# Kernel tuning notes

Hardware: AMD Instinct MI355X
Metric: run time of the kernel (lower is better)

## Reference

```python
import jax, jax.numpy as jnp
import numpy as np

B, C, H, W = 256, 256, 16, 16   # batch, backbone channels, spatial (H*W = 256 = loop count)
E, NCLS = 128, 200              # opt.embed_size, opt.class_num

def _conv(x, w, stride, pad):
    # NCHW / OIHW conv, explicit torch-style symmetric padding
    return jax.lax.conv_general_dilated(x, w, (stride, stride), [(pad, pad), (pad, pad)],
                                        dimension_numbers=('NCHW', 'OIHW', 'NCHW'))

def _bn(x, s, b):
    # eval-mode BatchNorm folded to per-channel scale + shift
    return x * s[None, :, None, None] + b[None, :, None, None]

def setup_inputs() -> dict:
    key = jax.random.key(0)
    ks = jax.random.split(key, 12)
    f = lambda k, shape, scale: jax.random.normal(k, shape, jnp.float32) * scale
    bn_s = lambda k, n: 1.0 + 0.05 * jax.random.normal(k, (n,), jnp.float32)
    bn_b = lambda k, n: 0.05 * jax.random.normal(k, (n,), jnp.float32)
    return {
        'x': f(ks[0], (B, C, H, W), 1.0),
        'embed_w': f(ks[1], (E, C), 0.05),
        'embed_b': f(ks[2], (E,), 0.05),
        'b1_conv1': f(ks[3], (512, 256, 3, 3), 0.03),
        'b1_bn1_s': bn_s(jax.random.fold_in(key, 101), 512),
        'b1_bn1_b': bn_b(jax.random.fold_in(key, 102), 512),
        'b1_conv2': f(ks[4], (512, 512, 3, 3), 0.02),
        'b1_bn2_s': bn_s(jax.random.fold_in(key, 103), 512),
        'b1_bn2_b': bn_b(jax.random.fold_in(key, 104), 512),
        'b1_down_w': f(ks[5], (512, 256, 1, 1), 0.05),
        'b1_down_s': bn_s(jax.random.fold_in(key, 105), 512),
        'b1_down_b': bn_b(jax.random.fold_in(key, 106), 512),
        'b2_conv1': f(ks[6], (512, 512, 3, 3), 0.02),
        'b2_bn1_s': bn_s(jax.random.fold_in(key, 107), 512),
        'b2_bn1_b': bn_b(jax.random.fold_in(key, 108), 512),
        'b2_conv2': f(ks[7], (512, 512, 3, 3), 0.02),
        'b2_bn2_s': bn_s(jax.random.fold_in(key, 109), 512),
        'b2_bn2_b': bn_b(jax.random.fold_in(key, 110), 512),
        'head_w': f(ks[8], (NCLS, 512), 0.05),
    }

def reference(x, embed_w, embed_b,
              b1_conv1, b1_bn1_s, b1_bn1_b, b1_conv2, b1_bn2_s, b1_bn2_b,
              b1_down_w, b1_down_s, b1_down_b,
              b2_conv1, b2_bn1_s, b2_bn1_b, b2_conv2, b2_bn2_s, b2_bn2_b,
              head_w):
    # --- resblock = resnet layer4 (two BasicBlocks, 256->512, stride 2) ---
    y = jax.nn.relu(_bn(_conv(x, b1_conv1, 2, 1), b1_bn1_s, b1_bn1_b))
    y = _bn(_conv(y, b1_conv2, 1, 1), b1_bn2_s, b1_bn2_b)
    sc = _bn(_conv(x, b1_down_w, 2, 0), b1_down_s, b1_down_b)
    y = jax.nn.relu(y + sc)                              # [B,512,8,8]
    z = jax.nn.relu(_bn(_conv(y, b2_conv1, 1, 1), b2_bn1_s, b2_bn1_b))
    z = _bn(_conv(z, b2_conv2, 1, 1), b2_bn2_s, b2_bn2_b)
    z = jax.nn.relu(z + y)
    # --- class prediction: global avg pool + bias-free linear ---
    feat = jnp.mean(z, axis=(2, 3))                      # [B,512]
    prediction = feat @ head_w.T                         # [B,NCLS]
    # --- consistency: 1x1-conv embedding, then pairwise Gram + sigmoid ---
    emb = jnp.einsum('bchw,ec->behw', x, embed_w) + embed_b[None, :, None, None]
    emb = emb.reshape(B, E, H * W)                       # [B,E,256]
    inv_sqrt_e = jnp.float32(1.0 / np.sqrt(E))
    # vol[b,q,i] = sum_c emb[b,c,i]*emb[b,c,q] / sqrt(E)  (matches the 256-iter loop)
    vol = jax.nn.sigmoid(jnp.einsum('bei,beq->bqi', emb, emb) * inv_sqrt_e)
    return (prediction, vol)
```

## Files before the change

kernel.cpp:

```cpp
#include <hip/hip_runtime.h>


using short8 = __attribute__((ext_vector_type(8))) short;
using f32x4  = __attribute__((ext_vector_type(4))) float;
typedef unsigned short u16;
typedef unsigned int   u32;

#define MFMA(a,b,c) __builtin_amdgcn_mfma_f32_16x16x32_bf16((a),(b),(c),0,0,0)

__device__ __forceinline__ u16 f2b(float f){
    u32 u = __builtin_bit_cast(u32, f);
    u += 0x7FFFu + ((u >> 16) & 1u);
    return (u16)(u >> 16);
}
__device__ __forceinline__ float b2f(u16 h){
    u32 u = ((u32)h) << 16;
    return __builtin_bit_cast(float, u);
}
__device__ __forceinline__ u32 pack2(float a, float b){
    return (u32)f2b(a) | ((u32)f2b(b) << 16);
}
__device__ __forceinline__ float sigmoidf_(float v){
    return 1.0f / (1.0f + __expf(-v));
}

__global__ __launch_bounds__(256)
void prep_kernel(const float* __restrict__ w1, const float* __restrict__ s1,
                 const float* __restrict__ w2, const float* __restrict__ s2,
                 const float* __restrict__ w3, const float* __restrict__ s3,
                 const float* __restrict__ w4, const float* __restrict__ s4,
                 const float* __restrict__ wd, const float* __restrict__ sd,
                 const float* __restrict__ ew,
                 u16* __restrict__ wp1, u16* __restrict__ wp2,
                 u16* __restrict__ wp3, u16* __restrict__ wp4,
                 u16* __restrict__ wpd, u16* __restrict__ wpe)
{
    const int N2 = 9*16*512*40, N1 = 9*8*512*40, ND = 8*512*40, NE = 8*128*40;
    int t = blockIdx.x * 256 + threadIdx.x;
    if (t < N2) {
        int j = t % 40; int r = t / 40; int co = r & 511; int q = r >> 9;
        int cc = q & 15; int dydx = q >> 4;
        float v = (j < 32) ? w2[(co*512 + cc*32 + j)*9 + dydx] * s2[co] : 0.f;
        wp2[t] = f2b(v); return;
    }
    t -= N2;
    if (t < N2) {
        int j = t % 40; int r = t / 40; int co = r & 511; int q = r >> 9;
        int cc = q & 15; int dydx = q >> 4;
        float v = (j < 32) ? w3[(co*512 + cc*32 + j)*9 + dydx] * s3[co] : 0.f;
        wp3[t] = f2b(v); return;
    }
    t -= N2;
    if (t < N2) {
        int j = t % 40; int r = t / 40; int co = r & 511; int q = r >> 9;
        int cc = q & 15; int dydx = q >> 4;
        float v = (j < 32) ? w4[(co*512 + cc*32 + j)*9 + dydx] * s4[co] : 0.f;
        wp4[t] = f2b(v); return;
    }
    t -= N2;
    if (t < N1) {
        int j = t % 40; int r = t / 40; int co = r & 511; int q = r >> 9;
        int cc = q & 7; int dydx = q >> 3;
        float v = (j < 32) ? w1[(co*256 + cc*32 + j)*9 + dydx] * s1[co] : 0.f;
        wp1[t] = f2b(v); return;
    }
    t -= N1;
    if (t < ND) {
        int j = t % 40; int r = t / 40; int co = r & 511; int cc = r >> 9;
        float v = (j < 32) ? wd[co*256 + cc*32 + j] * sd[co] : 0.f;
        wpd[t] = f2b(v); return;
    }
    t -= ND;
    if (t < NE) {
        int j = t % 40; int r = t / 40; int e = r & 127; int cc = r >> 7;
        float v = (j < 32) ? ew[e*256 + cc*32 + j] : 0.f;
        wpe[t] = f2b(v);
    }
}

__global__ __launch_bounds__(512, 2)
void conv1_kernel(const float* __restrict__ x, const u16* __restrict__ wp,
                  const float* __restrict__ bnb, u16* __restrict__ out)
{
    const int cot = blockIdx.x;
    const int b0  = blockIdx.y * 2;
    const int tid = threadIdx.x;
    const int wid = tid >> 6, lane = tid & 63;
    const int ln = lane & 15, kg = lane >> 4;
    const int wco = wid >> 1;
    const int bb  = wid & 1;

    __shared__ u16 actb[2][2*289*40];

    {
        short8 zz = {0,0,0,0,0,0,0,0};
        short8* ab = (short8*)&actb[0][0];
        for (int j = tid; j < 2*2*289*40/8; j += 512) ab[j] = zz;
    }
    __syncthreads();

    auto stage_act = [&](int cc, int p){
        #pragma unroll
        for (int it = 0; it < 16; ++it){
            int f = it*512 + tid;
            int bb2 = f >> 12; int rem = f & 4095;
            int cip = rem >> 8; int px = rem & 255;
            const float* src = &x[(((size_t)(b0+bb2)*256 + cc*32 + 2*cip)*256) + px];
            float v0 = src[0], v1 = src[256];
            int r = ((px >> 4) + 1)*17 + (px & 15) + 1;
            *(u32*)&actb[p][(bb2*289 + r)*40 + 2*cip] = pack2(v0, v1);
        }
    };

    stage_act(0, 0);
    __syncthreads();

    f32x4 zero4 = {0.f,0.f,0.f,0.f};
    f32x4 acc[4][4];
    #pragma unroll
    for (int mf = 0; mf < 4; ++mf)
        #pragma unroll
        for (int nf = 0; nf < 4; ++nf) acc[mf][nf] = zero4;

    int bbase[4];
    #pragma unroll
    for (int nf = 0; nf < 4; ++nf){
        int px = nf*16 + ln;
        bbase[nf] = (bb*289 + 34*(px>>3) + 2*(px&7))*40 + kg*8;
    }

    for (int cc = 0; cc < 8; ++cc){
        if (cc < 7) stage_act(cc+1, (cc+1) & 1);
        const u16* abp = actb[cc & 1];
        #pragma unroll
        for (int d = 0; d < 9; ++d){
            const u16* wdp = wp + ((size_t)(d*8 + cc)*512 + cot*256)*40;
            int dy = d/3, dx = d - dy*3;
            int shift = (dy*17 + dx)*40;
            short8 A[4];
            #pragma unroll
            for (int mf = 0; mf < 4; ++mf)
                A[mf] = *(const short8*)&wdp[(wco*64 + mf*16 + ln)*40 + kg*8];
            #pragma unroll
            for (int nf = 0; nf < 4; ++nf){
                short8 B = *(const short8*)&abp[bbase[nf] + shift];
                #pragma unroll
                for (int mf = 0; mf < 4; ++mf)
                    acc[mf][nf] = MFMA(A[mf], B, acc[mf][nf]);
            }
        }
        __syncthreads();
    }

    #pragma unroll
    for (int mf = 0; mf < 4; ++mf){
        int co0 = cot*256 + wco*64 + mf*16 + kg*4;
        float4 bv = *(const float4*)&bnb[co0];
        #pragma unroll
        for (int nf = 0; nf < 4; ++nf){
            int px = nf*16 + ln;
            size_t o = (((size_t)(b0+bb)*64) + px)*512 + co0;
            f32x4 a = acc[mf][nf];
            ushort4 st;
            st.x = f2b(fmaxf(a[0] + bv.x, 0.f));
            st.y = f2b(fmaxf(a[1] + bv.y, 0.f));
            st.z = f2b(fmaxf(a[2] + bv.z, 0.f));
            st.w = f2b(fmaxf(a[3] + bv.w, 0.f));
            *(ushort4*)&out[o] = st;
        }
    }
}

template<int DOWN, int RES>
__global__ __launch_bounds__(128, 3)
void conv_s1_kernel(const u16* __restrict__ in, const u16* __restrict__ wp,
                    const float* __restrict__ bnb,
                    const float* __restrict__ x, const u16* __restrict__ wpd,
                    const float* __restrict__ dbb,
                    const u16* __restrict__ res, u16* __restrict__ out)
{
    const int b   = blockIdx.x;
    const int cot = blockIdx.y;
    const int tid = threadIdx.x;
    const int wid = tid >> 6;
    const int lane = tid & 63;
    const int ln = lane & 15, kg = lane >> 4;

    __shared__ u16 actb[2][100*40];

    {
        short8 zz = {0,0,0,0,0,0,0,0};
        short8* ab = (short8*)&actb[0][0];
        for (int j = tid; j < 2*100*40/8; j += 128) ab[j] = zz;
    }
    __syncthreads();

    const int j0 = tid, j1 = 128 + tid;
    const int px0 = j0 >> 2, cg0 = j0 & 3;
    const int px1 = j1 >> 2, cg1 = j1 & 3;
    const int ld0 = (((px0>>3)+1)*10 + (px0&7) + 1)*40 + cg0*8;
    const int ld1 = (((px1>>3)+1)*10 + (px1&7) + 1)*40 + cg1*8;

    short8 sreg0, sreg1;
    auto stage_load = [&](int cc){
        sreg0 = *(const short8*)&in[(((size_t)b*64 + px0)*512) + cc*32 + cg0*8];
        sreg1 = *(const short8*)&in[(((size_t)b*64 + px1)*512) + cc*32 + cg1*8];
    };
    auto stage_store = [&](int p){
        *(short8*)&actb[p][ld0] = sreg0;
        *(short8*)&actb[p][ld1] = sreg1;
    };

    stage_load(0); stage_store(0);
    __syncthreads();

    f32x4 zero4 = {0.f,0.f,0.f,0.f};
    f32x4 acc[4][4];
    #pragma unroll
    for (int mf = 0; mf < 4; ++mf)
        #pragma unroll
        for (int nf = 0; nf < 4; ++nf) acc[mf][nf] = zero4;

    int bro[4];
    #pragma unroll
    for (int nf = 0; nf < 4; ++nf){
        int px = nf*16 + ln;
        bro[nf] = ((px>>3)*10 + (px&7))*40 + kg*8;
    }
    const int aoff = ln*40 + kg*8;
    const int abase = (cot*128 + wid*64)*40;

    for (int cc = 0; cc < 16; ++cc){
        if (cc < 15) stage_load(cc+1);
        const u16* abp = actb[cc & 1];
        #pragma unroll
        for (int dy = 0; dy < 3; ++dy){
            short8 A[3][4];
            #pragma unroll
            for (int dx = 0; dx < 3; ++dx){
                const u16* wdp = wp + (size_t)((dy*3+dx)*16 + cc)*512*40 + abase;
                #pragma unroll
                for (int mf = 0; mf < 4; ++mf)
                    A[dx][mf] = *(const short8*)&wdp[mf*640 + aoff];
            }
            #pragma unroll
            for (int dx = 0; dx < 3; ++dx){
                int shift = (dy*10 + dx)*40;
                #pragma unroll
                for (int nf = 0; nf < 4; ++nf){
                    short8 B = *(const short8*)&abp[bro[nf] + shift];
                    #pragma unroll
                    for (int mf = 0; mf < 4; ++mf)
                        acc[mf][nf] = MFMA(A[dx][mf], B, acc[mf][nf]);
                }
            }
        }
        if (cc < 15){
            stage_store((cc+1) & 1);
            __syncthreads();
        }
    }

    if (DOWN){
        for (int dc = 0; dc < 8; ++dc){
            __syncthreads();
            #pragma unroll
            for (int it = 0; it < 8; ++it){
                int f = it*128 + tid;
                int cip = f >> 6, px2 = f & 63;
                int ipx = (px2>>3)*32 + (px2&7)*2;
                const float* src = &x[(((size_t)b*256 + dc*32 + 2*cip)*256) + ipx];
                *(u32*)&actb[0][px2*40 + cip*2] = pack2(src[0], src[256]);
            }
            __syncthreads();
            const u16* wdp = wpd + (size_t)(dc*512)*40 + abase;
            short8 A[4];
            #pragma unroll
            for (int mf = 0; mf < 4; ++mf)
                A[mf] = *(const short8*)&wdp[mf*640 + aoff];
            #pragma unroll
            for (int nf = 0; nf < 4; ++nf){
                int rd = nf*16 + ln;
                short8 B = *(const short8*)&actb[0][rd*40 + kg*8];
                #pragma unroll
                for (int mf = 0; mf < 4; ++mf)
                    acc[mf][nf] = MFMA(A[mf], B, acc[mf][nf]);
            }
        }
    }

    #pragma unroll
    for (int mf = 0; mf < 4; ++mf){
        int co0 = cot*128 + wid*64 + mf*16 + kg*4;
        float4 bv = *(const float4*)&bnb[co0];
        if (DOWN){
            float4 dv = *(const float4*)&dbb[co0];
            bv.x += dv.x; bv.y += dv.y; bv.z += dv.z; bv.w += dv.w;
        }
        #pragma unroll
        for (int nf = 0; nf < 4; ++nf){
            int px = nf*16 + ln;
            size_t o = (((size_t)b*64) + px)*512 + co0;
            f32x4 a = acc[mf][nf];
            float v0 = a[0] + bv.x, v1 = a[1] + bv.y;
            float v2 = a[2] + bv.z, v3 = a[3] + bv.w;
            if (RES){
                ushort4 rv = *(const ushort4*)&res[o];
                v0 += b2f(rv.x); v1 += b2f(rv.y); v2 += b2f(rv.z); v3 += b2f(rv.w);
            }
            ushort4 st;
            st.x = f2b(fmaxf(v0, 0.f)); st.y = f2b(fmaxf(v1, 0.f));
            st.z = f2b(fmaxf(v2, 0.f)); st.w = f2b(fmaxf(v3, 0.f));
            *(ushort4*)&out[o] = st;
        }
    }
}

__global__ __launch_bounds__(256)
void head_kernel(const u16* __restrict__ z, const float* __restrict__ hw,
                 float* __restrict__ pred)
{
    const int b = blockIdx.x, tid = threadIdx.x;
    __shared__ float feat[512];
    float s0 = 0.f, s1 = 0.f;
    for (int px = 0; px < 64; ++px){
        u32 u = *(const u32*)&z[(((size_t)b*64 + px)*512) + 2*tid];
        s0 += b2f((u16)(u & 0xFFFF));
        s1 += b2f((u16)(u >> 16));
    }
    feat[2*tid]   = s0 * (1.f/64.f);
    feat[2*tid+1] = s1 * (1.f/64.f);
    __syncthreads();
    if (tid < 200){
        float acc = 0.f;
        const float4* hp = (const float4*)&hw[(size_t)tid*512];
        #pragma unroll 8
        for (int i = 0; i < 128; ++i){
            float4 h = hp[i];
            float4 f = *(const float4*)&feat[i*4];
            acc += h.x*f.x + h.y*f.y + h.z*f.z + h.w*f.w;
        }
        pred[b*200 + tid] = acc;
    }
}

__global__ __launch_bounds__(512, 2)
void gram_kernel(const float* __restrict__ x, const u16* __restrict__ wpe,
                 const float* __restrict__ eb, float* __restrict__ vol)
{
    const int b = blockIdx.x, tid = threadIdx.x;
    const int wid = tid >> 6, lane = tid & 63;
    const int ln = lane & 15, kg = lane >> 4;

    __shared__ u16 embl[256*136];
    __shared__ u16 xbl[256*40];
    __shared__ u16 ewl[128*40];

    f32x4 zero4 = {0.f,0.f,0.f,0.f};
    f32x4 ae[8][2];
    #pragma unroll
    for (int mf = 0; mf < 8; ++mf){ ae[mf][0] = zero4; ae[mf][1] = zero4; }

    for (int cc = 0; cc < 8; ++cc){
        __syncthreads();
        #pragma unroll
        for (int it = 0; it < 8; ++it){
            int f = it*512 + tid;
            int cip = f >> 8, px = f & 255;
            const float* src = &x[(((size_t)b*256 + cc*32 + 2*cip)*256) + px];
            *(u32*)&xbl[px*40 + 2*cip] = pack2(src[0], src[256]);
        }
        for (int j = tid; j < 640; j += 512)
            *(short8*)&ewl[j*8] = *(const short8*)&wpe[(cc*128)*40 + j*8];
        __syncthreads();
        short8 A[8];
        #pragma unroll
        for (int mf = 0; mf < 8; ++mf)
            A[mf] = *(const short8*)&ewl[(mf*16 + ln)*40 + kg*8];
        #pragma unroll
        for (int nf = 0; nf < 2; ++nf){
            short8 B = *(const short8*)&xbl[(wid*32 + nf*16 + ln)*40 + kg*8];
            #pragma unroll
            for (int mf = 0; mf < 8; ++mf)
                ae[mf][nf] = MFMA(A[mf], B, ae[mf][nf]);
        }
    }
    #pragma unroll
    for (int mf = 0; mf < 8; ++mf){
        int e0 = mf*16 + kg*4;
        float4 bv = *(const float4*)&eb[e0];
        #pragma unroll
        for (int nf = 0; nf < 2; ++nf){
            int px = wid*32 + nf*16 + ln;
            f32x4 a = ae[mf][nf];
            ushort4 st;
            st.x = f2b(a[0] + bv.x); st.y = f2b(a[1] + bv.y);
            st.z = f2b(a[2] + bv.z); st.w = f2b(a[3] + bv.w);
            *(ushort4*)&embl[px*136 + e0] = st;
        }
    }
    __syncthreads();

    const int wq = wid >> 2, wi = wid & 3;
    f32x4 g[8][4];
    #pragma unroll
    for (int mf = 0; mf < 8; ++mf)
        #pragma unroll
        for (int nf = 0; nf < 4; ++nf) g[mf][nf] = zero4;

    #pragma unroll
    for (int ks = 0; ks < 4; ++ks){
        short8 A[8];
        #pragma unroll
        for (int mf = 0; mf < 8; ++mf)
            A[mf] = *(const short8*)&embl[(wq*128 + mf*16 + ln)*136 + ks*32 + kg*8];
        #pragma unroll
        for (int nf = 0; nf < 4; ++nf){
            short8 B = *(const short8*)&embl[(wi*64 + nf*16 + ln)*136 + ks*32 + kg*8];
            #pragma unroll
            for (int mf = 0; mf < 8; ++mf)
                g[mf][nf] = MFMA(A[mf], B, g[mf][nf]);
        }
    }
    const float sc = 0.08838834764831845f;
    #pragma unroll
    for (int mf = 0; mf < 8; ++mf){
        #pragma unroll
        for (int nf = 0; nf < 4; ++nf){
            int i = wi*64 + nf*16 + ln;
            #pragma unroll
            for (int r = 0; r < 4; ++r){
                int q = wq*128 + mf*16 + kg*4 + r;
                vol[(((size_t)b*256 + q)*256) + i] = sigmoidf_(g[mf][nf][r] * sc);
            }
        }
    }
}

extern "C" void kernel_launch(void* const* d_in, const int* in_sizes, int n_in,
                              void* d_out, int out_size, void* d_ws, size_t ws_size,
                              hipStream_t stream)
{
    const float* x    = (const float*)d_in[0];
    const float* ew   = (const float*)d_in[1];
    const float* eb   = (const float*)d_in[2];
    const float* w1   = (const float*)d_in[3];
    const float* bn1s = (const float*)d_in[4];
    const float* bn1b = (const float*)d_in[5];
    const float* w2   = (const float*)d_in[6];
    const float* bn2s = (const float*)d_in[7];
    const float* bn2b = (const float*)d_in[8];
    const float* wd   = (const float*)d_in[9];
    const float* bnds = (const float*)d_in[10];
    const float* bndb = (const float*)d_in[11];
    const float* w3   = (const float*)d_in[12];
    const float* bn3s = (const float*)d_in[13];
    const float* bn3b = (const float*)d_in[14];
    const float* w4   = (const float*)d_in[15];
    const float* bn4s = (const float*)d_in[16];
    const float* bn4b = (const float*)d_in[17];
    const float* hw   = (const float*)d_in[18];

    float* pred = (float*)d_out;
    float* vol  = pred + 51200;

    u16* wp2 = (u16*)d_ws;
    u16* wp3 = wp2 + 2949120;
    u16* wp4 = wp3 + 2949120;
    u16* wp1 = wp4 + 2949120;
    u16* wpd = wp1 + 1474560;
    u16* wpe = wpd + 163840;

    u16* y1 = (u16*)vol;
    u16* y  = y1 + 8388608;
    u16* z1 = y  + 8388608;
    u16* z  = z1 + 8388608;

    prep_kernel<<<41120, 256, 0, stream>>>(w1, bn1s, w2, bn2s, w3, bn3s, w4, bn4s,
                                           wd, bnds, ew, wp1, wp2, wp3, wp4, wpd, wpe);
    conv1_kernel<<<dim3(2,128), 512, 0, stream>>>(x, wp1, bn1b, y1);
    conv_s1_kernel<1,0><<<dim3(256,4), 128, 0, stream>>>(y1, wp2, bn2b, x, wpd, bndb,
                                                         nullptr, y);
    conv_s1_kernel<0,0><<<dim3(256,4), 128, 0, stream>>>(y, wp3, bn3b, nullptr, nullptr,
                                                         nullptr, nullptr, z1);
    conv_s1_kernel<0,1><<<dim3(256,4), 128, 0, stream>>>(z1, wp4, bn4b, nullptr, nullptr,
                                                         nullptr, y, z);
    head_kernel<<<256, 256, 0, stream>>>(z, hw, pred);
    gram_kernel<<<256, 512, 0, stream>>>(x, wpe, eb, vol);
}
```

Measured before the change: 426.8 us.

## Use single-wave blocks for stride-1 convs and drop block barriers

Shrinks each stride-1 conv block from two waves to one wave covering 64 output channels, and doubles the grid's channel dimension to match. With a single wavefront per block, all __syncthreads barriers around the LDS double buffer and the downsample staging are removed. Each lane now stages four activation vectors per channel chunk instead of two. The cost is that each block re-stages the same activation tile that was previously shared by two waves, doubling LDS fill work and global activation reads. It also relies on intra-wave ordering of LDS writes and reads without explicit barriers.

New measurement: 400.4 us. 6.2% less time.

```diff
diff --git a/kernel.cpp b/kernel.cpp
--- a/kernel.cpp
+++ b/kernel.cpp
@@ -172,7 +172,7 @@
 }
 
 template<int DOWN, int RES>
-__global__ __launch_bounds__(128, 3)
+__global__ __launch_bounds__(64, 2)
 void conv_s1_kernel(const u16* __restrict__ in, const u16* __restrict__ wp,
                     const float* __restrict__ bnb,
                     const float* __restrict__ x, const u16* __restrict__ wpd,
@@ -181,9 +181,7 @@
 {
     const int b   = blockIdx.x;
     const int cot = blockIdx.y;
-    const int tid = threadIdx.x;
-    const int wid = tid >> 6;
-    const int lane = tid & 63;
+    const int lane = threadIdx.x;
     const int ln = lane & 15, kg = lane >> 4;
 
     __shared__ u16 actb[2][100*40];
@@ -191,28 +189,35 @@
     {
         short8 zz = {0,0,0,0,0,0,0,0};
         short8* ab = (short8*)&actb[0][0];
-        for (int j = tid; j < 2*100*40/8; j += 128) ab[j] = zz;
-    }
-    __syncthreads();
-
-    const int j0 = tid, j1 = 128 + tid;
-    const int px0 = j0 >> 2, cg0 = j0 & 3;
-    const int px1 = j1 >> 2, cg1 = j1 & 3;
-    const int ld0 = (((px0>>3)+1)*10 + (px0&7) + 1)*40 + cg0*8;
-    const int ld1 = (((px1>>3)+1)*10 + (px1&7) + 1)*40 + cg1*8;
-
-    short8 sreg0, sreg1;
+        #pragma unroll
+        for (int it = 0; it < 16; ++it){
+            int j = it*64 + lane;
+            if (j < 1000) ab[j] = zz;
+        }
+    }
+
+    int s_ld[4]; size_t s_go[4];
+    #pragma unroll
+    for (int it = 0; it < 4; ++it){
+        int j = it*64 + lane;
+        int px = j >> 2, cg = j & 3;
+        s_ld[it] = (((px>>3)+1)*10 + (px&7) + 1)*40 + cg*8;
+        s_go[it] = (((size_t)b*64 + px)*512) + cg*8;
+    }
+
+    short8 sreg[4];
     auto stage_load = [&](int cc){
-        sreg0 = *(const short8*)&in[(((size_t)b*64 + px0)*512) + cc*32 + cg0*8];
-        sreg1 = *(const short8*)&in[(((size_t)b*64 + px1)*512) + cc*32 + cg1*8];
+        #pragma unroll
+        for (int it = 0; it < 4; ++it)
+            sreg[it] = *(const short8*)&in[s_go[it] + cc*32];
     };
     auto stage_store = [&](int p){
-        *(short8*)&actb[p][ld0] = sreg0;
-        *(short8*)&actb[p][ld1] = sreg1;
+        #pragma unroll
+        for (int it = 0; it < 4; ++it)
+            *(short8*)&actb[p][s_ld[it]] = sreg[it];
     };
 
     stage_load(0); stage_store(0);
-    __syncthreads();
 
     f32x4 zero4 = {0.f,0.f,0.f,0.f};
     f32x4 acc[4][4];
@@ -228,7 +233,7 @@
         bro[nf] = ((px>>3)*10 + (px&7))*40 + kg*8;
     }
     const int aoff = ln*40 + kg*8;
-    const int abase = (cot*128 + wid*64)*40;
+    const int abase = cot*64*40;
 
     for (int cc = 0; cc < 16; ++cc){
         if (cc < 15) stage_load(cc+1);
@@ -255,24 +260,19 @@
                 }
             }
         }
-        if (cc < 15){
-            stage_store((cc+1) & 1);
-            __syncthreads();
-        }
+        if (cc < 15) stage_store((cc+1) & 1);
     }
 
     if (DOWN){
         for (int dc = 0; dc < 8; ++dc){
-            __syncthreads();
-            #pragma unroll
-            for (int it = 0; it < 8; ++it){
-                int f = it*128 + tid;
+            #pragma unroll
+            for (int it = 0; it < 16; ++it){
+                int f = it*64 + lane;
                 int cip = f >> 6, px2 = f & 63;
                 int ipx = (px2>>3)*32 + (px2&7)*2;
                 const float* src = &x[(((size_t)b*256 + dc*32 + 2*cip)*256) + ipx];
                 *(u32*)&actb[0][px2*40 + cip*2] = pack2(src[0], src[256]);
             }
-            __syncthreads();
             const u16* wdp = wpd + (size_t)(dc*512)*40 + abase;
             short8 A[4];
             #pragma unroll
@@ -291,7 +291,7 @@
 
     #pragma unroll
     for (int mf = 0; mf < 4; ++mf){
-        int co0 = cot*128 + wid*64 + mf*16 + kg*4;
+        int co0 = cot*64 + mf*16 + kg*4;
         float4 bv = *(const float4*)&bnb[co0];
         if (DOWN){
             float4 dv = *(const float4*)&dbb[co0];
@@ -479,12 +479,12 @@
     prep_kernel<<<41120, 256, 0, stream>>>(w1, bn1s, w2, bn2s, w3, bn3s, w4, bn4s,
                                            wd, bnds, ew, wp1, wp2, wp3, wp4, wpd, wpe);
     conv1_kernel<<<dim3(2,128), 512, 0, stream>>>(x, wp1, bn1b, y1);
-    conv_s1_kernel<1,0><<<dim3(256,4), 128, 0, stream>>>(y1, wp2, bn2b, x, wpd, bndb,
-                                                         nullptr, y);
-    conv_s1_kernel<0,0><<<dim3(256,4), 128, 0, stream>>>(y, wp3, bn3b, nullptr, nullptr,
-                                                         nullptr, nullptr, z1);
-    conv_s1_kernel<0,1><<<dim3(256,4), 128, 0, stream>>>(z1, wp4, bn4b, nullptr, nullptr,
-                                                         nullptr, y, z);
+    conv_s1_kernel<1,0><<<dim3(256,8), 64, 0, stream>>>(y1, wp2, bn2b, x, wpd, bndb,
+                                                        nullptr, y);
+    conv_s1_kernel<0,0><<<dim3(256,8), 64, 0, stream>>>(y, wp3, bn3b, nullptr, nullptr,
+                                                        nullptr, nullptr, z1);
+    conv_s1_kernel<0,1><<<dim3(256,8), 64, 0, stream>>>(z1, wp4, bn4b, nullptr, nullptr,
+                                                        nullptr, y, z);
     head_kernel<<<256, 256, 0, stream>>>(z, hw, pred);
     gram_kernel<<<256, 512, 0, stream>>>(x, wpe, eb, vol);
 }
```
